# Kernel optimization log

Measured on AMD Instinct MI355X. Metric: run time of the kernel, lower is better.

The kernel has to match this reference:

```python
import jax, jax.numpy as jnp
import numpy as np

NEG_INF = -9e9  # matches torch code's -9000000000.0


def setup_inputs() -> dict:
    key = jax.random.key(0)
    ks = jax.random.split(key, 12)
    B, N, L = 128, 32, 36
    Ds, Dv, H = 512, 1024, 512
    span_embeddings = jax.random.normal(ks[0], (B, N, Ds), dtype=jnp.float32)
    image_embeddings = jax.random.normal(ks[1], (B, L, Dv), dtype=jnp.float32)
    span_mask = jax.random.randint(ks[2], (B, N), 0, 2).astype(jnp.float32)
    image_mask = jax.random.randint(ks[3], (B, L), 0, 2).astype(jnp.float32)
    # BilinearPairWiseClassifier weight: maps span dim -> image dim
    Wg = jax.random.normal(ks[4], (Ds, Dv), dtype=jnp.float32) / np.sqrt(Ds)
    # SimplePairWiseClassifier MLP on concat(first, second, first*second)
    W1 = jax.random.normal(ks[5], (3 * Ds, H), dtype=jnp.float32) / np.sqrt(3 * Ds)
    b1 = jnp.zeros((H,), dtype=jnp.float32)
    W2 = jax.random.normal(ks[6], (H, H), dtype=jnp.float32) / np.sqrt(H)
    b2 = jnp.zeros((H,), dtype=jnp.float32)
    W3 = jax.random.normal(ks[7], (H, 1), dtype=jnp.float32) / np.sqrt(H)
    b3 = jnp.zeros((1,), dtype=jnp.float32)
    return {
        "span_embeddings": span_embeddings,
        "image_embeddings": image_embeddings,
        "span_mask": span_mask,
        "image_mask": image_mask,
        "Wg": Wg, "W1": W1, "b1": b1, "W2": W2, "b2": b2, "W3": W3, "b3": b3,
    }


def reference(span_embeddings, image_embeddings, span_mask, image_mask,
              Wg, W1, b1, W2, b2, W3, b3):
    B, N, Ds = span_embeddings.shape
    L = image_embeddings.shape[1]

    # ---- score_grounding (vectorized B^2 loop) ----
    # mention_scores[b] = bilinear(first[b], second[b]); the off-diagonal
    # 'score' in the original loop recomputes the SAME thing (only the mask
    # varies with jdx), so one (B,N,L) tensor suffices.
    M = jnp.einsum('bnd,de,ble->bnl', span_embeddings, Wg, image_embeddings)  # (B,N,L)
    # pairwise mask over doc pairs (i uses span_mask, j uses image_mask)
    pm = span_mask[:, None, :, None] * image_mask[None, :, None, :]  # (B,B,N,L)
    pm = jnp.where(pm != 0, pm, NEG_INF)
    w = jax.nn.softmax(pm.reshape(B, B, N * L), axis=-1).reshape(B, B, N, L)
    sent_scores = jnp.einsum('inl,ijnl->ij', M, w)  # (B,B)

    # ---- score_text: all span pairs via combinations(range(N), 2) ----
    iu, ju = np.triu_indices(N, k=1)  # same order as itertools.combinations
    first = span_embeddings[:, iu]    # (B,P,Ds)
    second = span_embeddings[:, ju]   # (B,P,Ds)
    feat = jnp.concatenate([first, second, first * second], axis=-1)  # (B,P,3Ds)
    h = jax.nn.relu(feat @ W1 + b1)
    h = jax.nn.relu(h @ W2 + b2)
    text_scores = (h @ W3 + b3)[..., 0]  # (B,P)

    # ---- contrastive loss over sentence-score matrix ----
    loss = (-jnp.sum(jax.nn.log_softmax(sent_scores, axis=1))
            - jnp.sum(jax.nn.log_softmax(sent_scores.T, axis=1))) / B
    return loss, M, text_scores
```

## Files before the change

kernel.cpp:

```cpp
#include <hip/hip_runtime.h>

#define B_  128
#define N_  32
#define L_  36
#define DS  512
#define DV  1024
#define H_  512
#define P_  496
#define R_  63488
#define LSE_BLKS 128
#define FUSE_BLKS (R_ / 64)

typedef __attribute__((ext_vector_type(8))) short bf16x8;
typedef __attribute__((ext_vector_type(4))) float f32x4;

__device__ __forceinline__ ushort f2bf(float x){
  unsigned u = __builtin_bit_cast(unsigned, x);
  return (ushort)((u + 0x7FFFu + ((u >> 16) & 1u)) >> 16);
}
__device__ __forceinline__ float bf2f(ushort u){
  unsigned v = ((unsigned)u) << 16;
  return __builtin_bit_cast(float, v);
}

__device__ __forceinline__ bf16x8 pkmul(bf16x8 a, bf16x8 b){
  union { unsigned u[4]; bf16x8 v; } o;
  #pragma unroll
  for (int e = 0; e < 4; ++e){
    float p0 = bf2f((ushort)a[2*e])   * bf2f((ushort)b[2*e]);
    float p1 = bf2f((ushort)a[2*e+1]) * bf2f((ushort)b[2*e+1]);
    asm("v_cvt_pk_bf16_f32 %0, %1, %2" : "=v"(o.u[e]) : "v"(p0), "v"(p1));
  }
  return o.v;
}

__device__ __forceinline__ void gload16(const void* g, void* l){
  __builtin_amdgcn_global_load_lds((const __attribute__((address_space(1))) unsigned*)g,
                                   (__attribute__((address_space(3))) unsigned*)l, 16, 0, 0);
}

__device__ __forceinline__ float wave_sum(float v){
  #pragma unroll
  for (int m = 32; m >= 1; m >>= 1) v += __shfl_xor(v, m);
  return v;
}
__device__ __forceinline__ float wave_max(float v){
  #pragma unroll
  for (int m = 32; m >= 1; m >>= 1) v = fmaxf(v, __shfl_xor(v, m));
  return v;
}

#define SPAN_F4 524288
#define IMG_F4  1179648
#define CONV_BLKS ((SPAN_F4 + IMG_F4) / 256)
#define TR_BLKS   (512 * 5)
__global__ void prep_all(const float* __restrict__ span, const float* __restrict__ img,
                         const float* __restrict__ b3,
                         const float* __restrict__ Wg, const float* __restrict__ W1,
                         const float* __restrict__ W2,
                         const float* __restrict__ sm, const float* __restrict__ im,
                         ushort* __restrict__ spbf, ushort* __restrict__ imgbf,
                         float* __restrict__ text,
                         ushort* __restrict__ WgT, ushort* __restrict__ UVBT,
                         ushort* __restrict__ W1cT, ushort* __restrict__ W2T,
                         float* cnt_s, float* cnt_i, int* iu, int* ju, float* loss){
  __shared__ float tile[32][33];
  const int bid = blockIdx.x, tid = threadIdx.x;
  if (bid < CONV_BLKS){
    int idx = bid * 256 + tid;
    if (idx < R_) text[idx] = b3[0];
    const float* src; ushort* dst; int k;
    if (idx < SPAN_F4){ src = span; dst = spbf; k = idx; }
    else              { src = img;  dst = imgbf; k = idx - SPAN_F4; }
    float4 v = *(const float4*)&src[(size_t)k * 4];
    ushort4 o; o.x = f2bf(v.x); o.y = f2bf(v.y); o.z = f2bf(v.z); o.w = f2bf(v.w);
    *(ushort4*)&dst[(size_t)k * 4] = o;
  } else if (bid < CONV_BLKS + TR_BLKS){
    int b = bid - CONV_BLKS;
    int z = b >> 9, rem = b & 511;
    int bx = rem & 31, by = rem >> 5;
    const float* src; ushort* dst; int Nn;
    if      (z == 0){ src = Wg;            dst = WgT;            Nn = 1024; }
    else if (z == 1){ src = W1;            dst = UVBT;           Nn = 512;  }
    else if (z == 2){ src = W1 + 512*512;  dst = UVBT + 512*512; Nn = 512;  }
    else if (z == 3){ src = W1 + 1024*512; dst = W1cT;           Nn = 512;  }
    else            { src = W2;            dst = W2T;            Nn = 512;  }
    if (bx * 32 >= Nn) return;
    int n0 = bx * 32, k0 = by * 32;
    int x = tid & 31, y = tid >> 5;
    #pragma unroll
    for (int i = 0; i < 4; ++i) tile[y + 8*i][x] = src[(k0 + y + 8*i) * Nn + n0 + x];
    __syncthreads();
    if (z >= 3){
      #pragma unroll
      for (int i = 0; i < 4; ++i){
        int n = n0 + y + 8*i, k = k0 + x;
        dst[(n >> 4)*8192 + (k >> 3)*128 + (n & 15)*8 + (k & 7)] = f2bf(tile[x][y + 8*i]);
      }
    } else {
      #pragma unroll
      for (int i = 0; i < 4; ++i) dst[(n0 + y + 8*i) * 512 + k0 + x] = f2bf(tile[x][y + 8*i]);
    }
  } else {
    int t = (bid - CONV_BLKS - TR_BLKS) * 256 + tid;
    if (t < P_){
      int i = 0, rem = t, cnt = N_ - 1;
      while (rem >= cnt){ rem -= cnt; ++i; --cnt; }
      iu[t] = i; ju[t] = i + 1 + rem;
    }
    if (t < B_){
      float s = 0.f;
      for (int n = 0; n < N_; ++n) s += sm[t*N_ + n];
      cnt_s[t] = s;
    } else if (t < 2*B_){
      int j = t - B_;
      float s = 0.f;
      for (int l = 0; l < L_; ++l) s += im[j*L_ + l];
      cnt_i[j] = s;
    }
    if (t == 0) loss[0] = 0.f;
  }
}

#define LDSH 32768

__device__ __forceinline__ void mma256(const ushort* __restrict__ A,
                                       const ushort* __restrict__ BT,
                                       size_t m0, int n0, ushort* lds,
                                       f32x4 acc[8][4]){
  const int tid = threadIdx.x;
  const int wid = tid >> 6, lane = tid & 63;
  const int wr = wid >> 2, wc = wid & 3;
  const int quad = lane >> 4, fm = lane & 15;
  const int swz = ((fm >> 2) & 3) << 4;
  const int srow_base = (wid & 3) * 8 + ((wid & 4) << 5) + (lane >> 3);
  const int scol = (lane & 7) * 8;

  #define STAGE_BAND(kt_, q_) do {                                        \
    int row_ = srow_base + 32 * (q_);                                     \
    int cg_  = (kt_) * 64 + (scol ^ (((row_ >> 2) & 3) << 4));            \
    int ld_  = ((kt_) & 1) * LDSH + row_ * 64 + scol;                     \
    gload16(A + (m0 + row_) * 512 + cg_, lds + ld_);                      \
    gload16(BT + (size_t)(n0 + row_) * 512 + cg_, lds + 16384 + ld_);     \
  } while (0)

  STAGE_BAND(0, 0); STAGE_BAND(0, 1); STAGE_BAND(0, 2); STAGE_BAND(0, 3);
  STAGE_BAND(1, 0); STAGE_BAND(1, 1); STAGE_BAND(1, 2);

  #pragma unroll
  for (int kt = 0; kt < 8; ++kt){
    const ushort* bufA = lds + (kt & 1) * LDSH;
    const ushort* bufB = bufA + 16384;
    bf16x8 bg[4][2];
    #pragma unroll
    for (int q = 0; q < 4; ++q){
      if (q == 0){
        if (kt == 7) asm volatile("s_waitcnt vmcnt(0)" ::: "memory");
        else         asm volatile("s_waitcnt vmcnt(6)" ::: "memory");
      }
      __builtin_amdgcn_s_barrier();
      if (q == 0){ if (kt + 1 < 8) STAGE_BAND(kt + 1, 3); }
      else       { if (kt + 2 < 8) STAGE_BAND(kt + 2, q - 1); }
      bf16x8 af[2][2];
      #pragma unroll
      for (int mi = 0; mi < 2; ++mi)
        #pragma unroll
        for (int kk = 0; kk < 2; ++kk)
          af[mi][kk] = *(const bf16x8*)&bufA[(wr*128 + (2*q + mi)*16 + fm) * 64
                                             + ((kk*32 + quad*8) ^ swz)];
      if (q == 0){
        #pragma unroll
        for (int n = 0; n < 4; ++n)
          #pragma unroll
          for (int kk = 0; kk < 2; ++kk)
            bg[n][kk] = *(const bf16x8*)&bufB[(wc*64 + n*16 + fm) * 64
                                              + ((kk*32 + quad*8) ^ swz)];
      }
      asm volatile("s_waitcnt lgkmcnt(0)" ::: "memory");
      __builtin_amdgcn_sched_barrier(0);
      __builtin_amdgcn_s_setprio(1);
      #pragma unroll
      for (int kk = 0; kk < 2; ++kk)
        #pragma unroll
        for (int mi = 0; mi < 2; ++mi)
          #pragma unroll
          for (int n = 0; n < 4; ++n)
            acc[2*q + mi][n] = __builtin_amdgcn_mfma_f32_16x16x32_bf16(
                af[mi][kk], bg[n][kk], acc[2*q + mi][n], 0, 0, 0);
      __builtin_amdgcn_s_setprio(0);
    }
  }
  #undef STAGE_BAND
}

__global__ __launch_bounds__(512, 2) void span2_gemm(const ushort* __restrict__ A,
                                                     const ushort* __restrict__ BT2,
                                                     ushort* __restrict__ SG,
                                                     ushort* __restrict__ UV){
  __shared__ ushort lds[2 * LDSH];
  f32x4 acc[8][4] = {};
  size_t m0 = (size_t)(blockIdx.x & 15) * 256;
  int ng = (int)(blockIdx.x >> 4) * 256;
  mma256(A, BT2, m0, ng, lds, acc);
  const int tid = threadIdx.x, wid = tid >> 6, lane = tid & 63;
  const int wr = wid >> 2, wc = wid & 3, quad = lane >> 4, fm = lane & 15;
  if (ng < 1024){
    #pragma unroll
    for (int m = 0; m < 8; ++m)
      #pragma unroll
      for (int r = 0; r < 4; ++r){
        size_t row = m0 + wr*128 + m*16 + quad*4 + r;
        #pragma unroll
        for (int n = 0; n < 4; ++n){
          int col = ng + wc*64 + n*16 + fm;
          SG[row * 1024 + col] = f2bf(acc[m][n][r]);
        }
      }
  } else {
    const int nbase = ng - 1024;
    const int pcb = (nbase & 512) + ((((nbase >> 7) + (wc >> 1)) & 3) << 7)
                  + fm * 8 + (wc & 1) * 4;
    #pragma unroll
    for (int m = 0; m < 8; ++m)
      #pragma unroll
      for (int r = 0; r < 4; ++r){
        size_t row = m0 + wr*128 + m*16 + quad*4 + r;
        uint2 pk;
        asm("v_cvt_pk_bf16_f32 %0, %1, %2" : "=v"(pk.x) : "v"(acc[m][0][r]), "v"(acc[m][1][r]));
        asm("v_cvt_pk_bf16_f32 %0, %1, %2" : "=v"(pk.y) : "v"(acc[m][2][r]), "v"(acc[m][3][r]));
        *(uint2*)(UV + row * 1024 + pcb) = pk;
      }
  }
}

__global__ __launch_bounds__(256) void batched_m_mfma(const ushort* __restrict__ SGbf,
                                                      const ushort* __restrict__ imgbf,
                                                      const float* __restrict__ sm,
                                                      float* __restrict__ Mout,
                                                      float* __restrict__ Msum,
                                                      float* __restrict__ Mtot){
  const int b = blockIdx.x;
  const int tid = threadIdx.x, wid = tid >> 6, lane = tid & 63;
  const int quad = lane >> 4, fm = lane & 15;
  __shared__ float red[4][32][48];
  __shared__ float shr[4];
  f32x4 acc[2][3] = {};
  const int wk = wid * 256;
  const ushort* Ab = SGbf + (size_t)b * 32 * 1024;
  const ushort* Bb = imgbf + (size_t)b * 36 * 1024;
  #pragma unroll
  for (int ks = 0; ks < 8; ++ks){
    const int k = wk + ks * 32 + quad * 8;
    bf16x8 af[2], bg[3];
    af[0] = *(const bf16x8*)&Ab[(0*16 + fm) * 1024 + k];
    af[1] = *(const bf16x8*)&Ab[(1*16 + fm) * 1024 + k];
    bg[0] = *(const bf16x8*)&Bb[(0*16 + fm) * 1024 + k];
    bg[1] = *(const bf16x8*)&Bb[(1*16 + fm) * 1024 + k];
    bg[2] = *(const bf16x8*)&Bb[(2*16 + fm) * 1024 + k];
    #pragma unroll
    for (int i = 0; i < 2; ++i)
      #pragma unroll
      for (int j = 0; j < 3; ++j)
        acc[i][j] = __builtin_amdgcn_mfma_f32_16x16x32_bf16(af[i], bg[j], acc[i][j], 0, 0, 0);
  }
  #pragma unroll
  for (int i = 0; i < 2; ++i)
    #pragma unroll
    for (int j = 0; j < 3; ++j)
      #pragma unroll
      for (int r = 0; r < 4; ++r)
        red[wid][i*16 + quad*4 + r][j*16 + fm] = acc[i][j][r];
  __syncthreads();
  float tot = 0.f;
  #pragma unroll
  for (int q = 0; q < 5; ++q){
    int out = tid + 256 * q;
    if (out < N_*L_){
      int n = out / L_, l = out - n * L_;
      float v = red[0][n][l] + red[1][n][l] + red[2][n][l] + red[3][n][l];
      Mout[b * (N_*L_) + out] = v;
      tot += v;
    }
  }
  tot = wave_sum(tot);
  if (lane == 0) shr[wid] = tot;
  __syncthreads();
  if (tid == 0) Mtot[b] = shr[0] + shr[1] + shr[2] + shr[3];
  if (tid < L_){
    float s = 0.f;
    for (int n = 0; n < N_; ++n){
      float mv = red[0][n][tid] + red[1][n][tid] + red[2][n][tid] + red[3][n][tid];
      s += mv * sm[b*N_ + n];
    }
    Msum[b*L_ + tid] = s;
  }
}

__device__ void lse_loss_body(const float* __restrict__ Msum, const float* __restrict__ im,
                              const float* __restrict__ cnt_s, const float* __restrict__ cnt_i,
                              const float* __restrict__ Mtot, float* __restrict__ out,
                              int i, float* sh ){
  const int tid = threadIdx.x;
  const int t = tid & 127;
  const int w4 = tid >> 6, lane = tid & 63;
  float sr = 0.f, sc = 0.f;
  #pragma unroll 4
  for (int l = 0; l < L_; ++l){
    sr += Msum[i*L_ + l] * im[t*L_ + l];
    sc += Msum[t*L_ + l] * im[i*L_ + l];
  }
  const float dr = cnt_s[i] * cnt_i[t];
  const float vr = (dr != 0.f) ? (sr / dr) : (Mtot[i] * (1.f/(float)(N_*L_)));
  const float dc = cnt_s[t] * cnt_i[i];
  const float vc = (dc != 0.f) ? (sc / dc) : (Mtot[t] * (1.f/(float)(N_*L_)));

  float m = wave_max(vr);
  if (lane == 0) sh[w4] = m;
  __syncthreads();
  const float mr = fmaxf(sh[0], sh[1]);
  __syncthreads();
  float e = wave_sum(expf(vr - mr));
  if (lane == 0) sh[w4] = e;
  __syncthreads();
  const float ser = sh[0] + sh[1];
  __syncthreads();
  float rs = wave_sum(vr);
  if (lane == 0) sh[w4] = rs;
  __syncthreads();
  const float rst = sh[0] + sh[1];
  __syncthreads();
  float mc0 = wave_max(vc);
  if (lane == 0) sh[w4] = mc0;
  __syncthreads();
  const float mc = fmaxf(sh[0], sh[1]);
  __syncthreads();
  float ec = wave_sum(expf(vc - mc));
  if (lane == 0) sh[w4] = ec;
  __syncthreads();
  const float sec = sh[0] + sh[1];
  if (tid == 0){
    float contrib = (mr + logf(ser)) + (mc + logf(sec)) - 2.f * rst / (float)B_;
    atomicAdd(out, contrib);
  }
}

__global__ __launch_bounds__(256, 2) void gemm_fused(
    const ushort* __restrict__ spbf, const ushort* __restrict__ W1cT,
    const ushort* __restrict__ W2T, const ushort* __restrict__ UV,
    const float* __restrict__ b1, const float* __restrict__ b2,
    const float* __restrict__ W3, const float* __restrict__ b3,
    const int* __restrict__ iu, const int* __restrict__ ju,
    float* __restrict__ text,
    const float* __restrict__ Msum, const float* __restrict__ im,
    const float* __restrict__ cnt_s, const float* __restrict__ cnt_i,
    const float* __restrict__ Mtot, float* __restrict__ loss){
  __shared__ ushort panel[32768];
  __shared__ float  partial[4][64];

  if (blockIdx.x < LSE_BLKS){
    lse_loss_body(Msum, im, cnt_s, cnt_i, Mtot, loss, blockIdx.x, (float*)partial);
    return;
  }
  const size_t m0 = (size_t)(blockIdx.x - LSE_BLKS) * 64;
  const int tid = threadIdx.x, wid = tid >> 6, lane = tid & 63;
  const int wc = wid;
  const int quad = lane >> 4, fm = lane & 15;
  const int f7 = fm & 7;

  {
    int row = tid >> 2;
    int c0  = tid & 3;
    int row_g = (int)m0 + row;
    int b = row_g / P_, p = row_g - b * P_;
    const ushort* xr = spbf + (size_t)(b * N_ + iu[p]) * 512;
    const ushort* yr = spbf + (size_t)(b * N_ + ju[p]) * 512;
    ushort* pr = panel + row * 512;
    int r7 = row & 7;
    #pragma unroll
    for (int i = 0; i < 16; ++i){
      int ch = c0 + 4*i;
      bf16x8 x = *(const bf16x8*)&xr[ch*8];
      bf16x8 y = *(const bf16x8*)&yr[ch*8];
      *(bf16x8*)&pr[(ch ^ r7) * 8] = pkmul(x, y);
    }
  }
  const ushort* pB1 = W1cT + wc * 65536 + quad * 128 + fm * 8;
  const ushort* pB2 = W2T  + wc * 65536 + quad * 128 + fm * 8;
  const int ar0 = (0*16 + fm) * 512;
  const int ar1 = (1*16 + fm) * 512;
  const int ar2 = (2*16 + fm) * 512;
  const int ar3 = (3*16 + fm) * 512;

  __syncthreads();

  #define LOADB(P, D, kt_) {                                                    \
    _Pragma("unroll")                                                           \
    for (int n_ = 0; n_ < 8; ++n_)                                              \
      D[n_] = *(const bf16x8*)&(P)[n_ * 8192 + (kt_) * 512];                    \
  }
  #define ITER(AC, kt_, CUR, NXT, P) {                                          \
    if ((kt_) < 15) LOADB(P, NXT, (kt_) + 1);                                   \
    int c_ = ((((kt_) * 4 + quad) ^ f7) * 8);                                   \
    bf16x8 a0 = *(const bf16x8*)&panel[ar0 + c_];                               \
    bf16x8 a1 = *(const bf16x8*)&panel[ar1 + c_];                               \
    bf16x8 a2 = *(const bf16x8*)&panel[ar2 + c_];                               \
    bf16x8 a3 = *(const bf16x8*)&panel[ar3 + c_];                               \
    __builtin_amdgcn_s_setprio(1);                                              \
    _Pragma("unroll")                                                           \
    for (int n_ = 0; n_ < 8; ++n_){                                             \
      AC[0][n_] = __builtin_amdgcn_mfma_f32_16x16x32_bf16(a0, CUR[n_], AC[0][n_], 0, 0, 0); \
      AC[1][n_] = __builtin_amdgcn_mfma_f32_16x16x32_bf16(a1, CUR[n_], AC[1][n_], 0, 0, 0); \
      AC[2][n_] = __builtin_amdgcn_mfma_f32_16x16x32_bf16(a2, CUR[n_], AC[2][n_], 0, 0, 0); \
      AC[3][n_] = __builtin_amdgcn_mfma_f32_16x16x32_bf16(a3, CUR[n_], AC[3][n_], 0, 0, 0); \
    }                                                                           \
    __builtin_amdgcn_s_setprio(0);                                              \
  }

  f32x4 acc[4][8] = {};
  bf16x8 g0[8], g1[8];
  LOADB(pB1, g0, 0);
  #pragma unroll 1
  for (int it = 0; it < 8; ++it){
    ITER(acc, 2*it,     g0, g1, pB1);
    ITER(acc, 2*it + 1, g1, g0, pB1);
  }
  __syncthreads();
  LOADB(pB2, g0, 0);

  {
    float b1v[8];
    #pragma unroll
    for (int n = 0; n < 8; ++n) b1v[n] = b1[wc*128 + n*16 + fm];
    const int uvoff = wc*128 + fm*8;
    #pragma unroll
    for (int m = 0; m < 4; ++m)
      #pragma unroll
      for (int r = 0; r < 4; ++r){
        int rowL = m*16 + quad*4 + r;
        int row_g = (int)m0 + rowL;
        int b = row_g / P_, p = row_g - b * P_;
        bf16x8 uv8 = *(const bf16x8*)(UV + (size_t)(b * N_ + iu[p]) * 1024 + uvoff);
        bf16x8 vv8 = *(const bf16x8*)(UV + (size_t)(b * N_ + ju[p]) * 1024 + 512 + uvoff);
        ushort* pr = panel + rowL * 512;
        int r7 = rowL & 7;
        #pragma unroll
        for (int n = 0; n < 8; n += 2){
          float h0 = fmaxf(acc[m][n][r]   + bf2f((ushort)uv8[n])   + bf2f((ushort)vv8[n])   + b1v[n],   0.f);
          float h1 = fmaxf(acc[m][n+1][r] + bf2f((ushort)uv8[n+1]) + bf2f((ushort)vv8[n+1]) + b1v[n+1], 0.f);
          unsigned pk;
          asm("v_cvt_pk_bf16_f32 %0, %1, %2" : "=v"(pk) : "v"(h0), "v"(h1));
          int col0 = wc*128 + n*16 + fm;
          int col1 = col0 + 16;
          pr[((((col0 >> 3) ^ r7) << 3) + (col0 & 7))] = (ushort)pk;
          pr[((((col1 >> 3) ^ r7) << 3) + (col1 & 7))] = (ushort)(pk >> 16);
        }
      }
  }
  __syncthreads();

  f32x4 acc2[4][8] = {};
  #pragma unroll 1
  for (int it = 0; it < 8; ++it){
    ITER(acc2, 2*it,     g0, g1, pB2);
    ITER(acc2, 2*it + 1, g1, g0, pB2);
  }
  #undef ITER
  #undef LOADB

  {
    float w3v[8], b2v[8];
    #pragma unroll
    for (int n = 0; n < 8; ++n){
      int col = wc*128 + n*16 + fm;
      w3v[n] = W3[col]; b2v[n] = b2[col];
    }
    #pragma unroll
    for (int m = 0; m < 4; ++m)
      #pragma unroll
      for (int r = 0; r < 4; ++r){
        float s = 0.f;
        #pragma unroll
        for (int n = 0; n < 8; ++n){
          float h = fmaxf(acc2[m][n][r] + b2v[n], 0.f);
          s = fmaf(h, w3v[n], s);
        }
        s += __shfl_xor(s, 1); s += __shfl_xor(s, 2);
        s += __shfl_xor(s, 4); s += __shfl_xor(s, 8);
        if (fm == 0) partial[wc][m*16 + quad*4 + r] = s;
      }
  }
  __syncthreads();
  if (tid < 64)
    text[m0 + tid] = partial[0][tid] + partial[1][tid] + partial[2][tid]
                   + partial[3][tid] + b3[0];
}

extern "C" void kernel_launch(void* const* d_in, const int* in_sizes, int n_in,
                              void* d_out, int out_size, void* d_ws, size_t ws_size,
                              hipStream_t stream) {
  const float* span = (const float*)d_in[0];
  const float* img  = (const float*)d_in[1];
  const float* sm   = (const float*)d_in[2];
  const float* im   = (const float*)d_in[3];
  const float* Wg   = (const float*)d_in[4];
  const float* W1   = (const float*)d_in[5];
  const float* b1   = (const float*)d_in[6];
  const float* W2   = (const float*)d_in[7];
  const float* b2   = (const float*)d_in[8];
  const float* W3   = (const float*)d_in[9];
  const float* b3   = (const float*)d_in[10];

  float* out  = (float*)d_out;
  float* loss = out;
  float* Mout = out + 1;
  float* text = out + 1 + B_*N_*L_;

  ushort* wsu  = (ushort*)d_ws;
  ushort* Zbf  = wsu;
  ushort* h1bf = Zbf + (size_t)R_*512;
  ushort* UVbf = h1bf + (size_t)R_*512;
  ushort* SGbf = UVbf + (size_t)4096*1024;
  ushort* spbf = SGbf + (size_t)4096*1024;
  ushort* imgbf= spbf + 4096*512;
  ushort* BT2  = imgbf + (size_t)(B_*L_ + 12)*1024;
  ushort* WgT  = BT2;
  ushort* UVBT = BT2 + 1024*512;
  ushort* W1cT = UVBT + 1024*512;
  ushort* W2T  = W1cT + 512*512;
  float* Msum  = (float*)(W2T + 512*512);
  float* Mtot  = Msum + B_*L_;
  float* cnt_s = Mtot + B_;
  float* cnt_i = cnt_s + B_;
  int*   iu    = (int*)(cnt_i + B_);
  int*   ju    = iu + P_;

  prep_all<<<CONV_BLKS + TR_BLKS + 2, 256, 0, stream>>>(
      span, img, b3, Wg, W1, W2, sm, im,
      spbf, imgbf, text, WgT, UVBT, W1cT, W2T, cnt_s, cnt_i, iu, ju, loss);

  span2_gemm<<<128, 512, 0, stream>>>(spbf, BT2, SGbf, UVbf);

  batched_m_mfma<<<B_, 256, 0, stream>>>(SGbf, imgbf, sm, Mout, Msum, Mtot);

  gemm_fused<<<LSE_BLKS + FUSE_BLKS, 256, 0, stream>>>(
      spbf, W1cT, W2T, UVbf, b1, b2, W3, b3, iu, ju, text,
      Msum, im, cnt_s, cnt_i, Mtot, loss);
}
```

Baseline: 196.5 us.

## Shrink span2_gemm tile to 128x256 and double grid to 256 blocks

The span2 GEMM (4096x2048x512) now uses 128-row M tiles instead of 256, doubling the grid from 128 to 256 blocks so more of the MI355X's compute units get work. The K-loop is simplified to a whole-tile double-buffered stage with barriers before and after compute, and block IDs are remapped to group blocks that share N tiles. This trades lower per-block operand reuse and a simpler, less interleaved load pipeline for better CU occupancy and smaller register and LDS footprint.

```diff
diff --git a/kernel.cpp b/kernel.cpp
--- a/kernel.cpp
+++ b/kernel.cpp
@@ -122,94 +122,88 @@
   }
 }
 
-#define LDSH 32768
-
-__device__ __forceinline__ void mma256(const ushort* __restrict__ A,
-                                       const ushort* __restrict__ BT,
-                                       size_t m0, int n0, ushort* lds,
-                                       f32x4 acc[8][4]){
-  const int tid = threadIdx.x;
-  const int wid = tid >> 6, lane = tid & 63;
-  const int wr = wid >> 2, wc = wid & 3;
-  const int quad = lane >> 4, fm = lane & 15;
-  const int swz = ((fm >> 2) & 3) << 4;
-  const int srow_base = (wid & 3) * 8 + ((wid & 4) << 5) + (lane >> 3);
-  const int scol = (lane & 7) * 8;
-
-  #define STAGE_BAND(kt_, q_) do {                                        \
-    int row_ = srow_base + 32 * (q_);                                     \
-    int cg_  = (kt_) * 64 + (scol ^ (((row_ >> 2) & 3) << 4));            \
-    int ld_  = ((kt_) & 1) * LDSH + row_ * 64 + scol;                     \
-    gload16(A + (m0 + row_) * 512 + cg_, lds + ld_);                      \
-    gload16(BT + (size_t)(n0 + row_) * 512 + cg_, lds + 16384 + ld_);     \
-  } while (0)
-
-  STAGE_BAND(0, 0); STAGE_BAND(0, 1); STAGE_BAND(0, 2); STAGE_BAND(0, 3);
-  STAGE_BAND(1, 0); STAGE_BAND(1, 1); STAGE_BAND(1, 2);
-
-  #pragma unroll
-  for (int kt = 0; kt < 8; ++kt){
-    const ushort* bufA = lds + (kt & 1) * LDSH;
-    const ushort* bufB = bufA + 16384;
-    bf16x8 bg[4][2];
-    #pragma unroll
-    for (int q = 0; q < 4; ++q){
-      if (q == 0){
-        if (kt == 7) asm volatile("s_waitcnt vmcnt(0)" ::: "memory");
-        else         asm volatile("s_waitcnt vmcnt(6)" ::: "memory");
-      }
-      __builtin_amdgcn_s_barrier();
-      if (q == 0){ if (kt + 1 < 8) STAGE_BAND(kt + 1, 3); }
-      else       { if (kt + 2 < 8) STAGE_BAND(kt + 2, q - 1); }
-      bf16x8 af[2][2];
-      #pragma unroll
-      for (int mi = 0; mi < 2; ++mi)
-        #pragma unroll
-        for (int kk = 0; kk < 2; ++kk)
-          af[mi][kk] = *(const bf16x8*)&bufA[(wr*128 + (2*q + mi)*16 + fm) * 64
-                                             + ((kk*32 + quad*8) ^ swz)];
-      if (q == 0){
-        #pragma unroll
-        for (int n = 0; n < 4; ++n)
-          #pragma unroll
-          for (int kk = 0; kk < 2; ++kk)
-            bg[n][kk] = *(const bf16x8*)&bufB[(wc*64 + n*16 + fm) * 64
-                                              + ((kk*32 + quad*8) ^ swz)];
-      }
-      asm volatile("s_waitcnt lgkmcnt(0)" ::: "memory");
-      __builtin_amdgcn_sched_barrier(0);
-      __builtin_amdgcn_s_setprio(1);
-      #pragma unroll
-      for (int kk = 0; kk < 2; ++kk)
-        #pragma unroll
-        for (int mi = 0; mi < 2; ++mi)
-          #pragma unroll
-          for (int n = 0; n < 4; ++n)
-            acc[2*q + mi][n] = __builtin_amdgcn_mfma_f32_16x16x32_bf16(
-                af[mi][kk], bg[n][kk], acc[2*q + mi][n], 0, 0, 0);
-      __builtin_amdgcn_s_setprio(0);
-    }
-  }
-  #undef STAGE_BAND
-}
+#define S2_LDSA 8192
+#define S2_BUF  24576
 
 __global__ __launch_bounds__(512, 2) void span2_gemm(const ushort* __restrict__ A,
                                                      const ushort* __restrict__ BT2,
                                                      ushort* __restrict__ SG,
                                                      ushort* __restrict__ UV){
-  __shared__ ushort lds[2 * LDSH];
-  f32x4 acc[8][4] = {};
-  size_t m0 = (size_t)(blockIdx.x & 15) * 256;
-  int ng = (int)(blockIdx.x >> 4) * 256;
-  mma256(A, BT2, m0, ng, lds, acc);
+  __shared__ ushort lds[2 * S2_BUF];
+  const int bid0 = blockIdx.x;
+  const int bid = ((bid0 & 7) << 5) | (bid0 >> 3);
+  const size_t m0 = (size_t)(bid & 31) * 128;
+  const int ng = (bid >> 5) * 256;
   const int tid = threadIdx.x, wid = tid >> 6, lane = tid & 63;
-  const int wr = wid >> 2, wc = wid & 3, quad = lane >> 4, fm = lane & 15;
+  const int wr = wid >> 2, wc = wid & 3;
+  const int quad = lane >> 4, fm = lane & 15;
+  const int swz = ((fm >> 2) & 3) << 4;
+
+  #define S2_STAGE(kt_, dst_) do {                                          \
+    _Pragma("unroll")                                                       \
+    for (int i_ = 0; i_ < 6; ++i_){                                         \
+      int u_ = i_ * 512 + tid;                                              \
+      if (u_ < 1024){                                                       \
+        int row_ = u_ >> 3, ch_ = (u_ & 7) << 3;                            \
+        gload16(A + (m0 + row_) * 512 + (kt_) * 64                          \
+                  + (ch_ ^ (((row_ >> 2) & 3) << 4)),                       \
+                (dst_) + row_ * 64 + ch_);                                  \
+      } else {                                                              \
+        int v_ = u_ - 1024;                                                 \
+        int row_ = v_ >> 3, ch_ = (v_ & 7) << 3;                            \
+        gload16(BT2 + (size_t)(ng + row_) * 512 + (kt_) * 64                \
+                  + (ch_ ^ (((row_ >> 2) & 3) << 4)),                       \
+                (dst_) + S2_LDSA + row_ * 64 + ch_);                        \
+      }                                                                     \
+    }                                                                       \
+  } while (0)
+
+  f32x4 acc[4][4] = {};
+  S2_STAGE(0, lds);
+  S2_STAGE(1, lds + S2_BUF);
+  #pragma unroll 1
+  for (int kt = 0; kt < 8; ++kt){
+    if (kt < 7) asm volatile("s_waitcnt vmcnt(6)" ::: "memory");
+    else        asm volatile("s_waitcnt vmcnt(0)" ::: "memory");
+    __builtin_amdgcn_s_barrier();
+    const ushort* bufA = lds + (kt & 1) * S2_BUF;
+    const ushort* bufB = bufA + S2_LDSA;
+    bf16x8 af[4][2], bg[4][2];
+    #pragma unroll
+    for (int m = 0; m < 4; ++m)
+      #pragma unroll
+      for (int kk = 0; kk < 2; ++kk)
+        af[m][kk] = *(const bf16x8*)&bufA[(wr*64 + m*16 + fm) * 64
+                                          + ((kk*32 + quad*8) ^ swz)];
+    #pragma unroll
+    for (int n = 0; n < 4; ++n)
+      #pragma unroll
+      for (int kk = 0; kk < 2; ++kk)
+        bg[n][kk] = *(const bf16x8*)&bufB[(wc*64 + n*16 + fm) * 64
+                                          + ((kk*32 + quad*8) ^ swz)];
+    asm volatile("s_waitcnt lgkmcnt(0)" ::: "memory");
+    __builtin_amdgcn_sched_barrier(0);
+    __builtin_amdgcn_s_setprio(1);
+    #pragma unroll
+    for (int kk = 0; kk < 2; ++kk)
+      #pragma unroll
+      for (int m = 0; m < 4; ++m)
+        #pragma unroll
+        for (int n = 0; n < 4; ++n)
+          acc[m][n] = __builtin_amdgcn_mfma_f32_16x16x32_bf16(
+              af[m][kk], bg[n][kk], acc[m][n], 0, 0, 0);
+    __builtin_amdgcn_s_setprio(0);
+    __builtin_amdgcn_s_barrier();
+    if (kt + 2 < 8) S2_STAGE(kt + 2, lds + (kt & 1) * S2_BUF);
+  }
+  #undef S2_STAGE
+
   if (ng < 1024){
     #pragma unroll
-    for (int m = 0; m < 8; ++m)
+    for (int m = 0; m < 4; ++m)
       #pragma unroll
       for (int r = 0; r < 4; ++r){
-        size_t row = m0 + wr*128 + m*16 + quad*4 + r;
+        size_t row = m0 + wr*64 + m*16 + quad*4 + r;
         #pragma unroll
         for (int n = 0; n < 4; ++n){
           int col = ng + wc*64 + n*16 + fm;
@@ -217,14 +211,14 @@
         }
       }
   } else {
-    const int nbase = ng - 1024;
-    const int pcb = (nbase & 512) + ((((nbase >> 7) + (wc >> 1)) & 3) << 7)
+    const int ngp = ng - 1024;
+    const int pcb = (ngp & 512) + (((((ngp & 511) >> 7) + (wc >> 1)) & 3) << 7)
                   + fm * 8 + (wc & 1) * 4;
     #pragma unroll
-    for (int m = 0; m < 8; ++m)
+    for (int m = 0; m < 4; ++m)
       #pragma unroll
       for (int r = 0; r < 4; ++r){
-        size_t row = m0 + wr*128 + m*16 + quad*4 + r;
+        size_t row = m0 + wr*64 + m*16 + quad*4 + r;
         uint2 pk;
         asm("v_cvt_pk_bf16_f32 %0, %1, %2" : "=v"(pk.x) : "v"(acc[m][0][r]), "v"(acc[m][1][r]));
         asm("v_cvt_pk_bf16_f32 %0, %1, %2" : "=v"(pk.y) : "v"(acc[m][2][r]), "v"(acc[m][3][r]));
@@ -538,7 +532,7 @@
       span, img, b3, Wg, W1, W2, sm, im,
       spbf, imgbf, text, WgT, UVBT, W1cT, W2T, cnt_s, cnt_i, iu, ju, loss);
 
-  span2_gemm<<<128, 512, 0, stream>>>(spbf, BT2, SGbf, UVbf);
+  span2_gemm<<<256, 512, 0, stream>>>(spbf, BT2, SGbf, UVbf);
 
   batched_m_mfma<<<B_, 256, 0, stream>>>(SGbf, imgbf, sm, Mout, Msum, Mtot);
 
```

Result: faster. 190.1 us (-3.2%).
